# Optimization experiments

Hardware: AMD Instinct MI355X
Metric: run time of the kernel (lower is better)

The kernel has to match this reference:

```python
import jax, jax.numpy as jnp
import numpy as np

NS, NV = 16, 4          # scalar / vector multiplicities
MODES = 2               # spectral conv retained fourier modes
C_OUT = 40              # out irreps dim: 16 + 4*3 + 4*3
EPS = 1e-5


def setup_inputs() -> dict:
    key = jax.random.key(0)
    ks = jax.random.split(key, 10)
    T, N, E = 8, 10000, 32768
    x = jax.random.normal(ks[0], (T, N, 28), jnp.float32)
    edge_index = jax.random.randint(ks[1], (2, E), 0, N)
    edge_attr = jax.random.normal(ks[2], (T, E, 48), jnp.float32)
    edge_sh = jax.random.normal(ks[3], (T, E, 4), jnp.float32)
    s = 1.0 / np.sqrt(48.0)
    w_mlp1 = jax.random.normal(ks[4], (48, 48), jnp.float32) * s
    b_mlp1 = jnp.zeros((48,), jnp.float32)
    w_mlp2 = jax.random.normal(ks[5], (48, 416), jnp.float32) * s
    b_mlp2 = jnp.zeros((416,), jnp.float32)
    sc = 1.0 / (NS * NS)
    tc_wr = jax.random.uniform(ks[6], (NS, NS, MODES), jnp.float32) * sc
    tc_wi = jax.random.uniform(ks[7], (NS, NS, MODES), jnp.float32) * sc
    bn_gamma = jnp.ones((C_OUT,), jnp.float32)
    bn_beta = jnp.zeros((C_OUT,), jnp.float32)
    return dict(x=x, edge_index=edge_index, edge_attr=edge_attr, edge_sh=edge_sh,
                w_mlp1=w_mlp1, b_mlp1=b_mlp1, w_mlp2=w_mlp2, b_mlp2=b_mlp2,
                tc_wr=tc_wr, tc_wi=tc_wi, bn_gamma=bn_gamma, bn_beta=bn_beta)


def reference(x, edge_index, edge_attr, edge_sh,
              w_mlp1, b_mlp1, w_mlp2, b_mlp2,
              tc_wr, tc_wi, bn_gamma, bn_beta):
    T, N, _ = x.shape
    E = edge_index.shape[1]
    src, dst = edge_index[0], edge_index[1]

    # ---- SpectralConv1d over the time axis (scalar channels only) ----
    xs = x[:, :, :NS]                                   # [T,N,16]
    xf = jnp.fft.rfft(xs, axis=0)                       # [T//2+1,N,16] c64
    w = tc_wr + 1j * tc_wi                              # [16,16,M]
    low = jnp.einsum('tni,iom->tno', xf[:MODES], jnp.moveaxis(w, -1, 0).transpose(1, 2, 0)[..., :MODES]) if False else jnp.einsum('mni,iom->mno', xf[:MODES], w)
    out_ft = jnp.zeros((T // 2 + 1, N, NS), jnp.complex64).at[:MODES].set(low)
    x_scalar = jnp.fft.irfft(out_ft, n=T, axis=0)       # [T,N,16]

    # ---- edge MLP -> per-edge tensor-product weights [T,E,416] ----
    h = jax.nn.relu(edge_attr @ w_mlp1 + b_mlp1)
    ew = h @ w_mlp2 + b_mlp2

    # ---- gather source node features per edge ----
    xe = x[:, src]                                      # [T,E,28]
    s = xe[..., :NS]                                    # [T,E,16]
    v = xe[..., NS:].reshape(T, E, NV, 3)               # [T,E,4,3]
    sh0 = edge_sh[..., :1]                              # [T,E,1]
    sh1 = edge_sh[..., 1:4]                             # [T,E,3]

    # path weight splits: 0e*0e->0e | 0e*1o->1o | 1o*0e->1o | 1o*1o->0e | 1o*1o->1e
    w00 = ew[..., 0:256].reshape(T, E, NS, NS)
    w01 = ew[..., 256:320].reshape(T, E, NS, NV)
    w10 = ew[..., 320:336].reshape(T, E, NV, NV)
    w110 = ew[..., 336:400].reshape(T, E, NV, NS)
    w111 = ew[..., 400:416].reshape(T, E, NV, NV)

    inv3 = 1.0 / np.sqrt(3.0)
    inv6 = 1.0 / np.sqrt(6.0)
    n0 = 1.0 / np.sqrt(20.0)   # fan-in norm for 0e output (16 + 4 paths)
    n1o = 1.0 / np.sqrt(20.0)  # fan-in norm for 1o output (16 + 4 paths)
    n1e = 1.0 / np.sqrt(4.0)   # fan-in norm for 1e output

    # scalar outputs
    p1 = jnp.einsum('tei,teio->teo', s * sh0, w00)
    vdots = jnp.einsum('teid,ted->tei', v, sh1) * inv3
    p4 = jnp.einsum('tei,teio->teo', vdots, w110)
    out0 = (p1 + p4) * n0                               # [T,E,16]

    # odd-vector outputs
    p2 = jnp.einsum('tei,teio->teo', s, w01)[..., None] * sh1[:, :, None, :] * inv3
    p3 = jnp.einsum('teid,teio->teod', v * sh0[..., None], w10) * inv3
    out1o = (p2 + p3) * n1o                             # [T,E,4,3]

    c = jnp.cross(v, sh1[:, :, None, :]) * inv6
    out1e = jnp.einsum('teid,teio->teod', c, w111) * n1e  # [T,E,4,3]

    msg = jnp.concatenate([out0,
                           out1o.reshape(T, E, NV * 3),
                           out1e.reshape(T, E, NV * 3)], axis=-1)  # [T,E,40]

    # ---- scatter_mean over destination nodes ----
    seg = jax.vmap(lambda m: jax.ops.segment_sum(m, dst, num_segments=N))(msg)
    cnt = jax.ops.segment_sum(jnp.ones((E,), msg.dtype), dst, num_segments=N)
    y = seg / jnp.maximum(cnt, 1.0)[None, :, None]      # [T,N,40]

    # ---- add spectral time-conv result to scalar channels ----
    y = jnp.concatenate([y[..., :NS] + x_scalar, y[..., NS:]], axis=-1)

    # ---- BatchNorm1d replicating torch permute/reshape semantics ----
    z = jnp.transpose(y, (1, 2, 0)).reshape(-1, C_OUT)  # [N*T, 40] (torch layout)
    mu = z.mean(axis=0)
    var = z.var(axis=0)
    z = (z - mu) / jnp.sqrt(var + EPS) * bn_gamma + bn_beta
    y = jnp.transpose(z.reshape(N, C_OUT, T), (2, 0, 1))
    return y
```

## Files before the change

### kernel.cpp

```cpp
#include <hip/hip_runtime.h>
#include <math.h>

#define TT 8
#define NN 10000
#define EE 32768
#define CC 40
#define EPSV 1e-05f

constexpr float INV3 = 0.57735026918962576f;
constexpr float INV6 = 0.40824829046386302f;
constexpr float N0F  = 0.22360679774997896f;
constexpr float N1OF = 0.22360679774997896f;
constexpr float N1EF = 0.5f;

constexpr float CTab[8] = {1.f, 0.70710678118654752f, 0.f, -0.70710678118654752f,
                           -1.f, -0.70710678118654752f, 0.f, 0.70710678118654752f};
constexpr float STab[8] = {0.f, 0.70710678118654752f, 1.f, 0.70710678118654752f,
                           0.f, -0.70710678118654752f, -1.f, -0.70710678118654752f};

typedef __attribute__((ext_vector_type(8))) short short8;
typedef __attribute__((ext_vector_type(4))) float f32x4;

__device__ __forceinline__ void atomAdd(float* p, float v) {
  __hip_atomic_fetch_add(p, v, __ATOMIC_RELAXED, __HIP_MEMORY_SCOPE_AGENT);
}

__device__ __forceinline__ short f2bfs(float f) {
  unsigned u = __builtin_bit_cast(unsigned, f);
  u = (u + 0x7fffu + ((u >> 16) & 1u)) >> 16;
  return (short)u;
}
__device__ __forceinline__ float bf2f(ushort u) {
  unsigned v = ((unsigned)u) << 16;
  return __builtin_bit_cast(float, v);
}

__global__ __launch_bounds__(256) void k_prep(const float* __restrict__ W1,
                                              const float* __restrict__ W2,
                                              short* __restrict__ W1F,
                                              short* __restrict__ W2F) {
  int idx = blockIdx.x * 256 + threadIdx.x;
  const int tot1 = 3 * 2 * 64 * 8;
  const int tot2 = 26 * 2 * 64 * 8;
  if (idx < tot1) {
    int elem = idx & 7, lane = (idx >> 3) & 63, kt = (idx >> 9) & 1, nt = idx >> 10;
    int j = kt * 32 + ((lane >> 4) << 2) + (elem & 3) + ((elem >> 2) << 4);
    int n = nt * 16 + (lane & 15);
    W1F[idx] = (j < 48) ? f2bfs(W1[j * 48 + n]) : (short)0;
  } else if (idx < tot1 + tot2) {
    int id2 = idx - tot1;
    int elem = id2 & 7, lane = (id2 >> 3) & 63, kt = (id2 >> 9) & 1, ck = id2 >> 10;
    int j = kt * 32 + ((lane >> 4) << 2) + (elem & 3) + ((elem >> 2) << 4);
    int n = ck * 16 + (lane & 15);
    W2F[id2] = (j < 48) ? f2bfs(W2[j * 416 + n]) : (short)0;
  }
}

__global__ __launch_bounds__(256) void k_spec(const float* __restrict__ x,
                                              const float* __restrict__ wr,
                                              const float* __restrict__ wi,
                                              float* __restrict__ xsc) {
  int gid = blockIdx.x * 256 + threadIdx.x;
  int n = gid >> 2, og = gid & 3;
  if (n >= NN) return;
  float F0[16], A[16], B[16];
#pragma unroll
  for (int i = 0; i < 16; ++i) { F0[i] = 0.f; A[i] = 0.f; B[i] = 0.f; }
#pragma unroll
  for (int t = 0; t < 8; ++t) {
    const float* xp = x + ((size_t)t * NN + n) * 28;
    const float ct = CTab[t], st = STab[t];
#pragma unroll
    for (int i = 0; i < 16; ++i) {
      float v = xp[i];
      F0[i] += v;
      A[i] = fmaf(v, ct, A[i]);
      B[i] = fmaf(v, -st, B[i]);
    }
  }
#pragma unroll
  for (int oo = 0; oo < 4; ++oo) {
    int o = og * 4 + oo;
    float r0 = 0.f, r1 = 0.f, i1 = 0.f;
#pragma unroll
    for (int i = 0; i < 16; ++i) {
      float wr0 = wr[i * 32 + o * 2 + 0];
      float wr1 = wr[i * 32 + o * 2 + 1];
      float wi1 = wi[i * 32 + o * 2 + 1];
      r0 = fmaf(F0[i], wr0, r0);
      r1 += A[i] * wr1 - B[i] * wi1;
      i1 += A[i] * wi1 + B[i] * wr1;
    }
#pragma unroll
    for (int t = 0; t < 8; ++t) {
      float val = 0.125f * (r0 + 2.f * (r1 * CTab[t] - i1 * STab[t]));
      xsc[((size_t)t * NN + n) * 16 + o] = val;
    }
  }
}

__global__ __launch_bounds__(256) void k_deg(const int* __restrict__ ei,
                                             int* __restrict__ deg) {
  int e = blockIdx.x * 256 + threadIdx.x;
  if (e >= EE) return;
  atomicAdd(&deg[ei[EE + e]], 1);
}

__global__ __launch_bounds__(1024) void k_scan(const int* __restrict__ deg,
                                               int* __restrict__ row_start,
                                               int* __restrict__ cursor) {
  __shared__ int sums[1024];
  int tid = threadIdx.x;
  const int PER = 10;
  int base = tid * PER;
  int s = 0;
#pragma unroll
  for (int i = 0; i < PER; ++i) {
    int idx = base + i;
    if (idx < NN) s += deg[idx];
  }
  sums[tid] = s;
  __syncthreads();
  for (int off = 1; off < 1024; off <<= 1) {
    int add = (tid >= off) ? sums[tid - off] : 0;
    __syncthreads();
    sums[tid] += add;
    __syncthreads();
  }
  int run = sums[tid] - s;
#pragma unroll
  for (int i = 0; i < PER; ++i) {
    int idx = base + i;
    if (idx < NN) {
      row_start[idx] = run;
      cursor[idx] = run;
      run += deg[idx];
    }
  }
  if (tid == 1023) row_start[NN] = run;
}

__global__ __launch_bounds__(256) void k_bucket(const int* __restrict__ ei,
                                                int* __restrict__ cursor,
                                                int* __restrict__ perm) {
  int e = blockIdx.x * 256 + threadIdx.x;
  if (e >= EE) return;
  int d = ei[EE + e];
  int slot = atomicAdd(&cursor[d], 1);
  perm[slot] = e;
}

__global__ __launch_bounds__(256, 4) void k_edge4(
    const float* __restrict__ x,
    const int* __restrict__ ei,
    const float* __restrict__ eag,
    const float* __restrict__ shg,
    const short* __restrict__ W1F,
    const short* __restrict__ W2F,
    const float* __restrict__ b1,
    const float* __restrict__ b2,
    ushort* __restrict__ msg)
{
  __shared__ float cSs[16][64];
  __shared__ float rawSs[16][64];
  __shared__ float cVDs[4][64];
  __shared__ float vS0s[12][64];
  __shared__ float sh1fs[3][64];
  __shared__ float cCRs[12][64];
  __shared__ ushort Hs[4][16][64];

  int blk = blockIdx.x;
  int t = blk >> 9;
  int e0 = (blk & 511) * 64;
  int tid = threadIdx.x;

  {
    int e = tid & 63;
    int role = tid >> 6;
    int eg = e0 + e;
    const float* shp = shg + ((size_t)t * EE + eg) * 4;
    float sh0 = shp[0], s1x = shp[1], s1y = shp[2], s1z = shp[3];
    int src = ei[eg];
    const float* xr = x + ((size_t)t * NN + src) * 28;
    const float F1 = INV3 * N1OF;
    if (role == 0) {
      sh1fs[0][e] = s1x * F1; sh1fs[1][e] = s1y * F1; sh1fs[2][e] = s1z * F1;
#pragma unroll
      for (int i = 0; i < 8; ++i) {
        float s = xr[i];
        rawSs[i][e] = s;
        cSs[i][e] = s * sh0 * N0F;
      }
    } else if (role == 1) {
#pragma unroll
      for (int i = 8; i < 16; ++i) {
        float s = xr[i];
        rawSs[i][e] = s;
        cSs[i][e] = s * sh0 * N0F;
      }
    } else {
      int i0 = (role == 2) ? 0 : 2;
#pragma unroll
      for (int ii = 0; ii < 2; ++ii) {
        int i = i0 + ii;
        float vx = xr[16 + 3 * i], vy = xr[17 + 3 * i], vz = xr[18 + 3 * i];
        cVDs[i][e] = (vx * s1x + vy * s1y + vz * s1z) * INV3 * N0F;
        vS0s[3 * i + 0][e] = vx * sh0 * F1;
        vS0s[3 * i + 1][e] = vy * sh0 * F1;
        vS0s[3 * i + 2][e] = vz * sh0 * F1;
        cCRs[3 * i + 0][e] = (vy * s1z - vz * s1y) * INV6 * N1EF;
        cCRs[3 * i + 1][e] = (vz * s1x - vx * s1z) * INV6 * N1EF;
        cCRs[3 * i + 2][e] = (vx * s1y - vy * s1x) * INV6 * N1EF;
      }
    }
  }
  __syncthreads();

  int w = tid >> 6, l = tid & 63;
  int col = l & 15;
  int kq  = (l >> 4) << 2;
  int eb  = w * 16;

  const float* row = eag + ((size_t)t * EE + e0 + eb + col) * 48;
  float4 fa = *(const float4*)(row + kq);
  float4 fb = *(const float4*)(row + 16 + kq);
  float4 fc = *(const float4*)(row + 32 + kq);
  short8 a0, a1;
  a0[0] = f2bfs(fa.x); a0[1] = f2bfs(fa.y); a0[2] = f2bfs(fa.z); a0[3] = f2bfs(fa.w);
  a0[4] = f2bfs(fb.x); a0[5] = f2bfs(fb.y); a0[6] = f2bfs(fb.z); a0[7] = f2bfs(fb.w);
  a1[0] = f2bfs(fc.x); a1[1] = f2bfs(fc.y); a1[2] = f2bfs(fc.z); a1[3] = f2bfs(fc.w);
  a1[4] = 0; a1[5] = 0; a1[6] = 0; a1[7] = 0;

  const short8* w1f = (const short8*)W1F;
  const short8* w2f = (const short8*)W2F;

#pragma unroll
  for (int nt = 0; nt < 3; ++nt) {
    float bias = b1[nt * 16 + col];
    f32x4 c = {bias, bias, bias, bias};
    c = __builtin_amdgcn_mfma_f32_16x16x32_bf16(a0, w1f[(nt * 2 + 0) * 64 + l], c, 0, 0, 0);
    c = __builtin_amdgcn_mfma_f32_16x16x32_bf16(a1, w1f[(nt * 2 + 1) * 64 + l], c, 0, 0, 0);
#pragma unroll
    for (int r = 0; r < 4; ++r) {
      int m = kq + r;
      float hv = fmaxf(c[r], 0.f);
      Hs[w][m][(nt * 16 + col) ^ ((m & 7) << 3)] = (ushort)f2bfs(hv);
    }
  }
#pragma unroll
  for (int r = 0; r < 4; ++r) {
    int m = kq + r;
    Hs[w][m][(48 + col) ^ ((m & 7) << 3)] = 0;
  }

  int m2 = col, X = (m2 & 7) << 3;
  ushort4 r0 = *(const ushort4*)&Hs[w][m2][(kq +  0) ^ X];
  ushort4 r1 = *(const ushort4*)&Hs[w][m2][(kq + 16) ^ X];
  ushort4 r2 = *(const ushort4*)&Hs[w][m2][(kq + 32) ^ X];
  ushort4 r3 = *(const ushort4*)&Hs[w][m2][(kq + 48) ^ X];
  short8 A20, A21;
  A20[0] = (short)r0.x; A20[1] = (short)r0.y; A20[2] = (short)r0.z; A20[3] = (short)r0.w;
  A20[4] = (short)r1.x; A20[5] = (short)r1.y; A20[6] = (short)r1.z; A20[7] = (short)r1.w;
  A21[0] = (short)r2.x; A21[1] = (short)r2.y; A21[2] = (short)r2.z; A21[3] = (short)r2.w;
  A21[4] = (short)r3.x; A21[5] = (short)r3.y; A21[6] = (short)r3.z; A21[7] = (short)r3.w;

  float acc0[4]  = {0.f, 0.f, 0.f, 0.f};
  float accP2[4] = {0.f, 0.f, 0.f, 0.f};
  float acc1o[3][4] = {{0.f,0.f,0.f,0.f},{0.f,0.f,0.f,0.f},{0.f,0.f,0.f,0.f}};
  float acc1e[3][4] = {{0.f,0.f,0.f,0.f},{0.f,0.f,0.f,0.f},{0.f,0.f,0.f,0.f}};
  int er0 = eb + kq;
  int iloc = col >> 2;
  int o = col & 3;

  short8 pf0[4], pf1[4];
#pragma unroll
  for (int i = 0; i < 4; ++i) {
    pf0[i] = w2f[(2 * i + 0) * 64 + l];
    pf1[i] = w2f[(2 * i + 1) * 64 + l];
  }

#pragma unroll
  for (int ck = 0; ck < 26; ++ck) {
    short8 B0 = pf0[ck & 3], B1 = pf1[ck & 3];
    if (ck + 4 < 26) {
      pf0[ck & 3] = w2f[(2 * (ck + 4) + 0) * 64 + l];
      pf1[ck & 3] = w2f[(2 * (ck + 4) + 1) * 64 + l];
    }
    float bias = b2[ck * 16 + col];
    f32x4 c = {bias, bias, bias, bias};
    c = __builtin_amdgcn_mfma_f32_16x16x32_bf16(A20, B0, c, 0, 0, 0);
    c = __builtin_amdgcn_mfma_f32_16x16x32_bf16(A21, B1, c, 0, 0, 0);

    if (ck < 16) {
#pragma unroll
      for (int r = 0; r < 4; ++r)
        acc0[r] = fmaf(cSs[ck][er0 + r], c[r], acc0[r]);
    } else if (ck < 20) {
#pragma unroll
      for (int r = 0; r < 4; ++r) {
        float q = rawSs[(ck - 16) * 4 + iloc][er0 + r] * c[r];
        q += __shfl_xor(q, 4);
        q += __shfl_xor(q, 8);
        accP2[r] += q;
      }
    } else if (ck == 20) {
#pragma unroll
      for (int d = 0; d < 3; ++d)
#pragma unroll
        for (int r = 0; r < 4; ++r) {
          float q = vS0s[iloc * 3 + d][er0 + r] * c[r];
          q += __shfl_xor(q, 4);
          q += __shfl_xor(q, 8);
          acc1o[d][r] += q;
        }
    } else if (ck < 25) {
#pragma unroll
      for (int r = 0; r < 4; ++r)
        acc0[r] = fmaf(cVDs[ck - 21][er0 + r], c[r], acc0[r]);
    } else {
#pragma unroll
      for (int d = 0; d < 3; ++d)
#pragma unroll
        for (int r = 0; r < 4; ++r) {
          float q = cCRs[iloc * 3 + d][er0 + r] * c[r];
          q += __shfl_xor(q, 4);
          q += __shfl_xor(q, 8);
          acc1e[d][r] += q;
        }
    }
  }

#pragma unroll
  for (int r = 0; r < 4; ++r) {
    size_t eg = (size_t)t * EE + e0 + er0 + r;
    msg[eg * 40 + col] = (ushort)f2bfs(acc0[r]);
  }
  if (col < 4) {
#pragma unroll
    for (int r = 0; r < 4; ++r) {
      int e = er0 + r;
      size_t eg = (size_t)t * EE + e0 + e;
      ushort* mrow = msg + eg * 40;
#pragma unroll
      for (int d = 0; d < 3; ++d) {
        mrow[16 + 3 * o + d] = (ushort)f2bfs(fmaf(accP2[r], sh1fs[d][e], acc1o[d][r]));
        mrow[28 + 3 * o + d] = (ushort)f2bfs(acc1e[d][r]);
      }
    }
  }
}

__global__ __launch_bounds__(320) void k_gather(const ushort* __restrict__ msg,
                                                const int* __restrict__ row_start,
                                                const int* __restrict__ perm,
                                                const float* __restrict__ xsc,
                                                float* __restrict__ out) {
  int tid = threadIdx.x;
  int blk = blockIdx.x;
  int t = blk / 1250;
  int nb = blk - t * 1250;
  int nloc = tid / 40, c = tid - nloc * 40;
  int n = nb * 8 + nloc;
  int a = row_start[n], b = row_start[n + 1];
  float acc = 0.f;
  for (int j = a; j < b; ++j) {
    int e = perm[j];
    acc += bf2f(msg[((size_t)t * EE + e) * 40 + c]);
  }
  float rc = 1.f / fmaxf((float)(b - a), 1.f);
  float y = acc * rc + (c < 16 ? xsc[((size_t)t * NN + n) * 16 + c] : 0.f);
  out[((size_t)t * NN + n) * 40 + c] = y;
}

__global__ __launch_bounds__(256) void k_stats(const float* __restrict__ out,
                                               float* __restrict__ stats) {
  int b = blockIdx.x;
  int t = b / 40;
  int chunk = b - t * 40;
  int n = chunk * 256 + threadIdx.x;
  float p[5] = {0.f, 0.f, 0.f, 0.f, 0.f};
  float q[5] = {0.f, 0.f, 0.f, 0.f, 0.f};
  if (n < NN) {
    const float* sp = out + ((size_t)t * NN + n) * 40;
#pragma unroll
    for (int c = 0; c < 40; ++c) {
      float y = sp[c];
      p[c % 5] += y;
      q[c % 5] = fmaf(y, y, q[c % 5]);
    }
  }
#pragma unroll
  for (int r = 0; r < 5; ++r) {
#pragma unroll
    for (int m = 32; m >= 1; m >>= 1) {
      p[r] += __shfl_xor(p[r], m);
      q[r] += __shfl_xor(q[r], m);
    }
  }
  __shared__ float ls[4][10];
  int lane = threadIdx.x & 63, wv = threadIdx.x >> 6;
  if (lane == 0) {
#pragma unroll
    for (int r = 0; r < 5; ++r) { ls[wv][r] = p[r]; ls[wv][5 + r] = q[r]; }
  }
  __syncthreads();
  if (threadIdx.x < 10) {
    int tid = threadIdx.x;
    float sum = ls[0][tid] + ls[1][tid] + ls[2][tid] + ls[3][tid];
    int r = tid % 5;
    int j = 8 * r + t;
    atomAdd(stats + (tid >= 5 ? 40 + j : j), sum);
  }
}

__global__ __launch_bounds__(256) void k_norm(const float* __restrict__ stats,
                                              const float* __restrict__ gam,
                                              const float* __restrict__ bet,
                                              float* __restrict__ out) {
  int idx4 = blockIdx.x * 256 + threadIdx.x;
  if (idx4 >= TT * NN * 10) return;
  int t = idx4 / (NN * 10);
  int rem = idx4 - t * NN * 10;
  int c0 = (rem % 10) * 4;
  const float inv = 1.f / (8.f * (float)NN);
  float4* op = (float4*)out;
  float4 y = op[idx4];
  float vals[4] = {y.x, y.y, y.z, y.w};
#pragma unroll
  for (int k = 0; k < 4; ++k) {
    int c = c0 + k;
    int j = 8 * (c % 5) + t;
    float mu = stats[j] * inv;
    float var = stats[40 + j] * inv - mu * mu;
    vals[k] = (vals[k] - mu) * rsqrtf(var + EPSV) * gam[j] + bet[j];
  }
  y.x = vals[0]; y.y = vals[1]; y.z = vals[2]; y.w = vals[3];
  op[idx4] = y;
}

extern "C" void kernel_launch(void* const* d_in, const int* in_sizes, int n_in,
                              void* d_out, int out_size, void* d_ws, size_t ws_size,
                              hipStream_t stream) {
  const float* x   = (const float*)d_in[0];
  const int*   ei  = (const int*)d_in[1];
  const float* ea  = (const float*)d_in[2];
  const float* esh = (const float*)d_in[3];
  const float* W1  = (const float*)d_in[4];
  const float* b1  = (const float*)d_in[5];
  const float* W2  = (const float*)d_in[6];
  const float* b2  = (const float*)d_in[7];
  const float* wr  = (const float*)d_in[8];
  const float* wi  = (const float*)d_in[9];
  const float* gam = (const float*)d_in[10];
  const float* bet = (const float*)d_in[11];
  float* out = (float*)d_out;

  float*  xsc       = (float*)d_ws;
  ushort* W1F       = (ushort*)(xsc + 1280000);
  ushort* W2F       = W1F + 3072;
  ushort* msg       = W2F + 26624;
  float*  stats     = (float*)(msg + (size_t)10485760);
  int*    deg       = (int*)(stats + 80);
  int*    cursor    = deg + 10000;
  int*    row_start = cursor + 10000;
  int*    perm      = row_start + 10001;

  hipMemsetAsync(stats, 0, (80 + 10000 + 10000) * sizeof(int), stream);

  k_prep<<<(29696 + 255) / 256, 256, 0, stream>>>(W1, W2, (short*)W1F, (short*)W2F);
  k_spec<<<(4 * NN + 255) / 256, 256, 0, stream>>>(x, wr, wi, xsc);
  k_deg<<<EE / 256, 256, 0, stream>>>(ei, deg);
  k_scan<<<1, 1024, 0, stream>>>(deg, row_start, cursor);
  k_bucket<<<EE / 256, 256, 0, stream>>>(ei, cursor, perm);
  k_edge4<<<TT * (EE / 64), 256, 0, stream>>>(x, ei, ea, esh, (short*)W1F, (short*)W2F,
                                              b1, b2, msg);
  k_gather<<<TT * 1250, 320, 0, stream>>>(msg, row_start, perm, xsc, out);
  k_stats<<<8 * 40, 256, 0, stream>>>(out, stats);
  k_norm<<<(TT * NN * 10 + 255) / 256, 256, 0, stream>>>(stats, gam, bet, out);
}
```

Before: 150.1 us.

## Merge prep/spectral/degree kernels and fuse gather with batchnorm statistics

```diff
diff --git a/kernel.cpp b/kernel.cpp
--- a/kernel.cpp
+++ b/kernel.cpp
@@ -35,82 +35,88 @@
   return __builtin_bit_cast(float, v);
 }
 
-__global__ __launch_bounds__(256) void k_prep(const float* __restrict__ W1,
-                                              const float* __restrict__ W2,
-                                              short* __restrict__ W1F,
-                                              short* __restrict__ W2F) {
-  int idx = blockIdx.x * 256 + threadIdx.x;
-  const int tot1 = 3 * 2 * 64 * 8;
-  const int tot2 = 26 * 2 * 64 * 8;
-  if (idx < tot1) {
-    int elem = idx & 7, lane = (idx >> 3) & 63, kt = (idx >> 9) & 1, nt = idx >> 10;
-    int j = kt * 32 + ((lane >> 4) << 2) + (elem & 3) + ((elem >> 2) << 4);
-    int n = nt * 16 + (lane & 15);
-    W1F[idx] = (j < 48) ? f2bfs(W1[j * 48 + n]) : (short)0;
-  } else if (idx < tot1 + tot2) {
-    int id2 = idx - tot1;
-    int elem = id2 & 7, lane = (id2 >> 3) & 63, kt = (id2 >> 9) & 1, ck = id2 >> 10;
-    int j = kt * 32 + ((lane >> 4) << 2) + (elem & 3) + ((elem >> 2) << 4);
-    int n = ck * 16 + (lane & 15);
-    W2F[id2] = (j < 48) ? f2bfs(W2[j * 416 + n]) : (short)0;
-  }
-}
-
-__global__ __launch_bounds__(256) void k_spec(const float* __restrict__ x,
-                                              const float* __restrict__ wr,
-                                              const float* __restrict__ wi,
-                                              float* __restrict__ xsc) {
-  int gid = blockIdx.x * 256 + threadIdx.x;
-  int n = gid >> 2, og = gid & 3;
-  if (n >= NN) return;
-  float F0[16], A[16], B[16];
-#pragma unroll
-  for (int i = 0; i < 16; ++i) { F0[i] = 0.f; A[i] = 0.f; B[i] = 0.f; }
-#pragma unroll
-  for (int t = 0; t < 8; ++t) {
-    const float* xp = x + ((size_t)t * NN + n) * 28;
-    const float ct = CTab[t], st = STab[t];
-#pragma unroll
-    for (int i = 0; i < 16; ++i) {
-      float v = xp[i];
-      F0[i] += v;
-      A[i] = fmaf(v, ct, A[i]);
-      B[i] = fmaf(v, -st, B[i]);
-    }
-  }
-#pragma unroll
-  for (int oo = 0; oo < 4; ++oo) {
-    int o = og * 4 + oo;
-    float r0 = 0.f, r1 = 0.f, i1 = 0.f;
-#pragma unroll
-    for (int i = 0; i < 16; ++i) {
-      float wr0 = wr[i * 32 + o * 2 + 0];
-      float wr1 = wr[i * 32 + o * 2 + 1];
-      float wi1 = wi[i * 32 + o * 2 + 1];
-      r0 = fmaf(F0[i], wr0, r0);
-      r1 += A[i] * wr1 - B[i] * wi1;
-      i1 += A[i] * wi1 + B[i] * wr1;
-    }
+#define SPEC_B 157
+#define DEG_B  128
+#define PREP_B 116
+__global__ __launch_bounds__(256) void k_pre(const float* __restrict__ x,
+                                             const float* __restrict__ wr,
+                                             const float* __restrict__ wi,
+                                             const int* __restrict__ ei,
+                                             const float* __restrict__ W1,
+                                             const float* __restrict__ W2,
+                                             float* __restrict__ xsc,
+                                             int* __restrict__ deg,
+                                             short* __restrict__ W1F,
+                                             short* __restrict__ W2F) {
+  int b = blockIdx.x, tid = threadIdx.x;
+  if (b < SPEC_B) {
+    int gid = b * 256 + tid;
+    int n = gid >> 2, og = gid & 3;
+    if (n >= NN) return;
+    float F0[16], A[16], B[16];
+#pragma unroll
+    for (int i = 0; i < 16; ++i) { F0[i] = 0.f; A[i] = 0.f; B[i] = 0.f; }
 #pragma unroll
     for (int t = 0; t < 8; ++t) {
-      float val = 0.125f * (r0 + 2.f * (r1 * CTab[t] - i1 * STab[t]));
-      xsc[((size_t)t * NN + n) * 16 + o] = val;
-    }
-  }
-}
-
-__global__ __launch_bounds__(256) void k_deg(const int* __restrict__ ei,
-                                             int* __restrict__ deg) {
-  int e = blockIdx.x * 256 + threadIdx.x;
-  if (e >= EE) return;
-  atomicAdd(&deg[ei[EE + e]], 1);
+      const float4* xp = (const float4*)(x + ((size_t)t * NN + n) * 28);
+      float4 v0 = xp[0], v1 = xp[1], v2 = xp[2], v3 = xp[3];
+      const float ct = CTab[t], st = STab[t];
+      float vv[16] = {v0.x, v0.y, v0.z, v0.w, v1.x, v1.y, v1.z, v1.w,
+                      v2.x, v2.y, v2.z, v2.w, v3.x, v3.y, v3.z, v3.w};
+#pragma unroll
+      for (int i = 0; i < 16; ++i) {
+        F0[i] += vv[i];
+        A[i] = fmaf(vv[i], ct, A[i]);
+        B[i] = fmaf(vv[i], -st, B[i]);
+      }
+    }
+#pragma unroll
+    for (int oo = 0; oo < 4; ++oo) {
+      int o = og * 4 + oo;
+      float r0 = 0.f, r1 = 0.f, i1 = 0.f;
+#pragma unroll
+      for (int i = 0; i < 16; ++i) {
+        float wr0 = wr[i * 32 + o * 2 + 0];
+        float wr1 = wr[i * 32 + o * 2 + 1];
+        float wi1 = wi[i * 32 + o * 2 + 1];
+        r0 = fmaf(F0[i], wr0, r0);
+        r1 += A[i] * wr1 - B[i] * wi1;
+        i1 += A[i] * wi1 + B[i] * wr1;
+      }
+#pragma unroll
+      for (int t = 0; t < 8; ++t) {
+        float val = 0.125f * (r0 + 2.f * (r1 * CTab[t] - i1 * STab[t]));
+        xsc[((size_t)t * NN + n) * 16 + o] = val;
+      }
+    }
+  } else if (b < SPEC_B + DEG_B) {
+    int e = (b - SPEC_B) * 256 + tid;
+    if (e < EE) atomicAdd(&deg[ei[EE + e]], 1);
+  } else {
+    int idx = (b - SPEC_B - DEG_B) * 256 + tid;
+    const int tot1 = 3 * 2 * 64 * 8;
+    if (idx < tot1) {
+      int elem = idx & 7, lane = (idx >> 3) & 63, kt = (idx >> 9) & 1, nt = idx >> 10;
+      int j = kt * 32 + ((lane >> 4) << 2) + (elem & 3) + ((elem >> 2) << 4);
+      int n = nt * 16 + (lane & 15);
+      W1F[idx] = (j < 48) ? f2bfs(W1[j * 48 + n]) : (short)0;
+    } else {
+      int id2 = idx - tot1;
+      int elem = id2 & 7, lane = (id2 >> 3) & 63, kt = (id2 >> 9) & 1, ck = id2 >> 10;
+      int j = kt * 32 + ((lane >> 4) << 2) + (elem & 3) + ((elem >> 2) << 4);
+      int n = ck * 16 + (lane & 15);
+      W2F[id2] = (j < 48) ? f2bfs(W2[j * 416 + n]) : (short)0;
+    }
+  }
 }
 
 __global__ __launch_bounds__(1024) void k_scan(const int* __restrict__ deg,
                                                int* __restrict__ row_start,
-                                               int* __restrict__ cursor) {
+                                               int* __restrict__ cursor,
+                                               float* __restrict__ stats) {
   __shared__ int sums[1024];
   int tid = threadIdx.x;
+  if (tid < 80) stats[tid] = 0.f;
   const int PER = 10;
   int base = tid * PER;
   int s = 0;
@@ -350,66 +356,45 @@
   }
 }
 
-__global__ __launch_bounds__(320) void k_gather(const ushort* __restrict__ msg,
+__global__ __launch_bounds__(320) void k_gstats(const ushort* __restrict__ msg,
                                                 const int* __restrict__ row_start,
                                                 const int* __restrict__ perm,
                                                 const float* __restrict__ xsc,
-                                                float* __restrict__ out) {
+                                                float* __restrict__ out,
+                                                float* __restrict__ stats) {
+  int blk = blockIdx.x;
+  int t = blk / 157;
+  int nb = blk - t * 157;
   int tid = threadIdx.x;
-  int blk = blockIdx.x;
-  int t = blk / 1250;
-  int nb = blk - t * 1250;
-  int nloc = tid / 40, c = tid - nloc * 40;
-  int n = nb * 8 + nloc;
-  int a = row_start[n], b = row_start[n + 1];
-  float acc = 0.f;
-  for (int j = a; j < b; ++j) {
-    int e = perm[j];
-    acc += bf2f(msg[((size_t)t * EE + e) * 40 + c]);
-  }
-  float rc = 1.f / fmaxf((float)(b - a), 1.f);
-  float y = acc * rc + (c < 16 ? xsc[((size_t)t * NN + n) * 16 + c] : 0.f);
-  out[((size_t)t * NN + n) * 40 + c] = y;
-}
-
-__global__ __launch_bounds__(256) void k_stats(const float* __restrict__ out,
-                                               float* __restrict__ stats) {
-  int b = blockIdx.x;
-  int t = b / 40;
-  int chunk = b - t * 40;
-  int n = chunk * 256 + threadIdx.x;
-  float p[5] = {0.f, 0.f, 0.f, 0.f, 0.f};
-  float q[5] = {0.f, 0.f, 0.f, 0.f, 0.f};
-  if (n < NN) {
-    const float* sp = out + ((size_t)t * NN + n) * 40;
-#pragma unroll
-    for (int c = 0; c < 40; ++c) {
-      float y = sp[c];
-      p[c % 5] += y;
-      q[c % 5] = fmaf(y, y, q[c % 5]);
-    }
-  }
-#pragma unroll
-  for (int r = 0; r < 5; ++r) {
-#pragma unroll
-    for (int m = 32; m >= 1; m >>= 1) {
-      p[r] += __shfl_xor(p[r], m);
-      q[r] += __shfl_xor(q[r], m);
-    }
-  }
-  __shared__ float ls[4][10];
-  int lane = threadIdx.x & 63, wv = threadIdx.x >> 6;
-  if (lane == 0) {
-#pragma unroll
-    for (int r = 0; r < 5; ++r) { ls[wv][r] = p[r]; ls[wv][5 + r] = q[r]; }
-  }
+  int g = tid / 40, c = tid - g * 40;
+  int r5 = c % 5;
+  __shared__ float sred[10];
+  if (tid < 10) sred[tid] = 0.f;
   __syncthreads();
-  if (threadIdx.x < 10) {
-    int tid = threadIdx.x;
-    float sum = ls[0][tid] + ls[1][tid] + ls[2][tid] + ls[3][tid];
+  float p = 0.f, q = 0.f;
+  for (int step = 0; step < 8; ++step) {
+    int n = nb * 64 + step * 8 + g;
+    if (n < NN) {
+      int a = row_start[n], b = row_start[n + 1];
+      float acc = 0.f;
+      for (int j = a; j < b; ++j) {
+        int e = perm[j];
+        acc += bf2f(msg[((size_t)t * EE + e) * 40 + c]);
+      }
+      float y = acc / fmaxf((float)(b - a), 1.f) +
+                (c < 16 ? xsc[((size_t)t * NN + n) * 16 + c] : 0.f);
+      out[((size_t)t * NN + n) * 40 + c] = y;
+      p += y;
+      q = fmaf(y, y, q);
+    }
+  }
+  atomicAdd(&sred[r5], p);
+  atomicAdd(&sred[5 + r5], q);
+  __syncthreads();
+  if (tid < 10) {
     int r = tid % 5;
     int j = 8 * r + t;
-    atomAdd(stats + (tid >= 5 ? 40 + j : j), sum);
+    atomAdd(stats + (tid >= 5 ? 40 + j : j), sred[tid]);
   }
 }
 
@@ -465,16 +450,14 @@
   int*    row_start = cursor + 10000;
   int*    perm      = row_start + 10001;
 
-  hipMemsetAsync(stats, 0, (80 + 10000 + 10000) * sizeof(int), stream);
-
-  k_prep<<<(29696 + 255) / 256, 256, 0, stream>>>(W1, W2, (short*)W1F, (short*)W2F);
-  k_spec<<<(4 * NN + 255) / 256, 256, 0, stream>>>(x, wr, wi, xsc);
-  k_deg<<<EE / 256, 256, 0, stream>>>(ei, deg);
-  k_scan<<<1, 1024, 0, stream>>>(deg, row_start, cursor);
+  hipMemsetAsync(deg, 0, 10000 * sizeof(int), stream);
+
+  k_pre<<<SPEC_B + DEG_B + PREP_B, 256, 0, stream>>>(x, wr, wi, ei, W1, W2, xsc, deg,
+                                                     (short*)W1F, (short*)W2F);
+  k_scan<<<1, 1024, 0, stream>>>(deg, row_start, cursor, stats);
   k_bucket<<<EE / 256, 256, 0, stream>>>(ei, cursor, perm);
   k_edge4<<<TT * (EE / 64), 256, 0, stream>>>(x, ei, ea, esh, (short*)W1F, (short*)W2F,
                                               b1, b2, msg);
-  k_gather<<<TT * 1250, 320, 0, stream>>>(msg, row_start, perm, xsc, out);
-  k_stats<<<8 * 40, 256, 0, stream>>>(out, stats);
+  k_gstats<<<TT * 157, 320, 0, stream>>>(msg, row_start, perm, xsc, out, stats);
   k_norm<<<(TT * NN * 10 + 255) / 256, 256, 0, stream>>>(stats, gam, bet, out);
 }
```

After: 158.5 us. 1.06x slower.
